# Kernel optimization log

Measured on AMD Instinct MI355X. Metric: run time of the kernel, lower is better.

Reference implementation:

```python
import jax, jax.numpy as jnp
import numpy as np

N = 50000          # num nodes
E = 800000         # num edges (avg degree 16)
C_IN = 64          # input channels
TOWERS = 4
F_IN = C_IN // TOWERS       # 16 (divide_input=True)
OUT = 128
F_OUT = OUT // TOWERS       # 32
NUM_AGG = 4                 # mean, std, max, min
NUM_SC = 3                  # identity, amplification, attenuation
AVG_LOG_DEG = float(np.log(17.0))  # deg histogram: all nodes degree 16 -> log(16+1)


def setup_inputs() -> dict:
    key = jax.random.key(0)
    ks = jax.random.split(key, 10)
    nodes = jax.random.normal(ks[0], (N, C_IN), dtype=jnp.float32)
    senders = jax.random.randint(ks[1], (E,), 0, N)
    receivers = jax.random.randint(ks[2], (E,), 0, N)
    # per-tower pre-MLP: Linear(2*F_IN -> F_IN), pre_layers=1 (no activation)
    pre_w = jax.random.normal(ks[3], (TOWERS, 2 * F_IN, F_IN), dtype=jnp.float32) / np.sqrt(2 * F_IN)
    pre_b = jnp.zeros((TOWERS, F_IN), dtype=jnp.float32)
    # per-tower post-MLP: Linear(F_IN + F_IN*12 -> F_OUT), post_layers=1
    post_in = F_IN + F_IN * NUM_AGG * NUM_SC  # 208
    post_w = jax.random.normal(ks[4], (TOWERS, post_in, F_OUT), dtype=jnp.float32) / np.sqrt(post_in)
    post_b = jnp.zeros((TOWERS, F_OUT), dtype=jnp.float32)
    # final linear: TOWERS*F_OUT -> OUT
    lin_w = jax.random.normal(ks[5], (TOWERS * F_OUT, OUT), dtype=jnp.float32) / np.sqrt(TOWERS * F_OUT)
    lin_b = jnp.zeros((OUT,), dtype=jnp.float32)
    return {"nodes": nodes, "senders": senders, "receivers": receivers,
            "pre_w": pre_w, "pre_b": pre_b, "post_w": post_w, "post_b": post_b,
            "lin_w": lin_w, "lin_b": lin_b}


def reference(nodes, senders, receivers, pre_w, pre_b, post_w, post_b, lin_w, lin_b):
    # divide_input=True: split channels across towers -> [N, T, F_IN]
    x = nodes.reshape(N, TOWERS, F_IN)
    x_i = x[senders]                                  # [E, T, F_IN]
    x_j = x[receivers]                                # [E, T, F_IN]
    h = jnp.concatenate([x_i, x_j], axis=-1)          # [E, T, 2*F_IN]
    # per-tower pre-MLP (single linear), vectorized over towers
    msg = jnp.einsum('etf,tfo->eto', h, pre_w) + pre_b  # [E, T, F_IN]

    # degree-scaled multi-aggregator segment reduce over receivers
    count = jax.ops.segment_sum(jnp.ones((E,), dtype=msg.dtype), receivers, num_segments=N)  # [N]
    d = jnp.clip(count, 1.0, None)
    inv_d = (1.0 / d)[:, None, None]
    mean = jax.ops.segment_sum(msg, receivers, num_segments=N) * inv_d           # [N,T,F]
    mean_sq = jax.ops.segment_sum(msg * msg, receivers, num_segments=N) * inv_d
    std = jnp.sqrt(jax.nn.relu(mean_sq - mean * mean) + 1e-5)
    has_nb = (count > 0)[:, None, None]
    mx = jax.ops.segment_max(msg, receivers, num_segments=N)
    mx = jnp.where(has_nb, mx, 0.0)
    mn = -jax.ops.segment_max(-msg, receivers, num_segments=N)
    mn = jnp.where(has_nb, mn, 0.0)
    agg = jnp.concatenate([mean, std, mx, mn], axis=-1)  # [N, T, 4*F_IN]

    # scalers: identity, amplification, attenuation (degree clamped to >= 1)
    log_d = jnp.log(d + 1.0)[:, None, None]
    amp = log_d / AVG_LOG_DEG
    att = AVG_LOG_DEG / log_d
    scaled = jnp.concatenate([agg, agg * amp, agg * att], axis=-1)  # [N, T, 12*F_IN]

    out = jnp.concatenate([x, scaled], axis=-1)                     # [N, T, 13*F_IN]
    outs = jnp.einsum('ntf,tfo->nto', out, post_w) + post_b         # [N, T, F_OUT]
    flat = outs.reshape(N, TOWERS * F_OUT)                          # [N, 128]
    return flat @ lin_w + lin_b                                     # [N, OUT]
```

## Files before the change

### kernel.cpp

```cpp
#include <hip/hip_runtime.h>

#define AVG_LOG_DEG 2.8332133440562162f
#define CAP 64

typedef __attribute__((ext_vector_type(8))) short short8;
typedef __attribute__((ext_vector_type(4))) float f32x4;

static __device__ __forceinline__ float bl(unsigned u) { return __uint_as_float(u << 16); }
static __device__ __forceinline__ float bh(unsigned u) { return __uint_as_float(u & 0xffff0000u); }
static __device__ __forceinline__ unsigned short f2b(float f) {
    unsigned u = __float_as_uint(f);
    return (unsigned short)((u + 0x7fffu + ((u >> 16) & 1u)) >> 16);
}
static __device__ __forceinline__ unsigned pk(unsigned short lo, unsigned short hi) {
    return (unsigned)lo | ((unsigned)hi << 16);
}


__global__ __launch_bounds__(256) void k_setup(
    const float* __restrict__ nodes, const float* __restrict__ pre_w,
    const float* __restrict__ post_w, const float* __restrict__ lin_w,
    float* __restrict__ Y, unsigned short* __restrict__ postT,
    unsigned short* __restrict__ linT, int* __restrict__ cursor,
    int n, int A, int nbN)
{
    int b = blockIdx.x;
    if (b < A) {
        int lane = threadIdx.x & 63;
        int node = b * 4 + (threadIdx.x >> 6);
        if (node >= n) return;
        int t = lane >> 4, f = lane & 15;
        float w[16];
        #pragma unroll
        for (int k = 0; k < 16; ++k)
            w[k] = pre_w[(t * 32 + k) * 16 + f];
        const float4* xp = reinterpret_cast<const float4*>(nodes + (size_t)node * 64 + t * 16);
        float4 x0 = xp[0], x1 = xp[1], x2 = xp[2], x3 = xp[3];
        float xs[16] = {x0.x, x0.y, x0.z, x0.w, x1.x, x1.y, x1.z, x1.w,
                        x2.x, x2.y, x2.z, x2.w, x3.x, x3.y, x3.z, x3.w};
        float y = 0.f;
        #pragma unroll
        for (int k = 0; k < 16; ++k)
            y = fmaf(xs[k], w[k], y);
        Y[(size_t)node * 64 + lane] = y;
    } else if (b < A + 176) {
        int i = (b - A) * 256 + threadIdx.x;
        if (i < 28672) {
            int t = i / (32 * 224);
            int r = i % (32 * 224);
            int nn = r / 224;
            int k = r % 224;
            float wv;
            if (k < 192)      wv = post_w[((size_t)t * 208 + 16 + k) * 32 + nn];
            else if (k < 208) wv = post_w[((size_t)t * 208 + (k - 192)) * 32 + nn];
            else              wv = 0.f;
            postT[i] = f2b(wv);
        }
        int j = i - 28672;
        if (j >= 0 && j < 16384) {
            int nn = j >> 7, k = j & 127;
            linT[j] = f2b(lin_w[k * 128 + nn]);
        }
    } else {
        int i = (b - A - 176) * 256 + threadIdx.x;
        if (i < n) cursor[i] = 0;
    }
}


__global__ __launch_bounds__(256) void k_scatter2(
    const int* __restrict__ send, const int* __restrict__ recv,
    int* __restrict__ cursor, int* __restrict__ slots,
    int e, int nps)
{
    int slice = blockIdx.x & 7;
    int chunk = blockIdx.x >> 3;
    int base = chunk * 2048;
    int lo = slice * nps;
    #pragma unroll
    for (int it = 0; it < 8; ++it) {
        int i = base + it * 256 + threadIdx.x;
        if (i < e) {
            int r = recv[i];
            if ((unsigned)(r - lo) < (unsigned)nps) {
                int p = atomicAdd(&cursor[r], 1);
                if (p < CAP) slots[(size_t)r * CAP + p] = send[i];
            }
        }
    }
}


__global__ __launch_bounds__(256) void k_agg(
    const float* __restrict__ nodes,
    const float* __restrict__ pre_w,
    const float* __restrict__ pre_b,
    const int* __restrict__ cursor,
    const int* __restrict__ slots, const float* __restrict__ Y,
    unsigned short* __restrict__ aggh, int n)
{
    int lane = threadIdx.x & 63;
    int node = blockIdx.x * 4 + (threadIdx.x >> 6);
    if (node >= n) return;
    int t = lane >> 4, f = lane & 15;

    int idxv = slots[(size_t)node * CAP + lane];

    float w[16];
    #pragma unroll
    for (int k = 0; k < 16; ++k)
        w[k] = pre_w[(t * 32 + 16 + k) * 16 + f];
    const float4* xp = reinterpret_cast<const float4*>(nodes + (size_t)node * 64 + t * 16);
    float4 x0 = xp[0], x1 = xp[1], x2 = xp[2], x3 = xp[3];
    float xs[16] = {x0.x, x0.y, x0.z, x0.w, x1.x, x1.y, x1.z, x1.w,
                    x2.x, x2.y, x2.z, x2.w, x3.x, x3.y, x3.z, x3.w};
    float hjw = pre_b[t * 16 + f];
    #pragma unroll
    for (int k = 0; k < 16; ++k)
        hjw = fmaf(xs[k], w[k], hjw);

    int d = min(cursor[node], CAP);
    const float* Yl = Y + lane;

    float s = 0.f, s2 = 0.f, mx = -INFINITY, mn = INFINITY;
    int e = 0;
    for (; e + 16 <= d; e += 16) {
        float v[16];
        #pragma unroll
        for (int q = 0; q < 16; ++q) {
            int si = __builtin_amdgcn_readlane(idxv, e + q);
            v[q] = Yl[(size_t)si * 64];
        }
        #pragma unroll
        for (int q = 0; q < 16; ++q) {
            float m = v[q] + hjw;
            s += m;
            s2 = fmaf(m, m, s2);
            mx = fmaxf(mx, m);
            mn = fminf(mn, m);
        }
    }
    int rem = d - e;
    if (rem > 0) {
        float v[16];
        #pragma unroll
        for (int q = 0; q < 16; ++q) {
            int si = __builtin_amdgcn_readlane(idxv, min(e + q, d - 1));
            v[q] = Yl[(size_t)si * 64];
        }
        #pragma unroll
        for (int q = 0; q < 16; ++q) {
            if (q < rem) {
                float m = v[q] + hjw;
                s += m;
                s2 = fmaf(m, m, s2);
                mx = fmaxf(mx, m);
                mn = fminf(mn, m);
            }
        }
    }

    float dc = fmaxf((float)d, 1.f);
    float inv = 1.f / dc;
    float mean = s * inv;
    float var = fmaf(-mean, mean, s2 * inv);
    float sd = sqrtf(fmaxf(var, 0.f) + 1e-5f);
    if (d == 0) { mx = 0.f; mn = 0.f; }

    unsigned short* ag = aggh + (size_t)node * 256 + t * 64 + f;
    ag[0]  = f2b(mean);
    ag[16] = f2b(sd);
    ag[32] = f2b(mx);
    ag[48] = f2b(mn);
}


__global__ __launch_bounds__(256, 3) void k_post(
    const float* __restrict__ nodes,
    const unsigned short* __restrict__ aggh,
    const int* __restrict__ deg,
    const unsigned short* __restrict__ postT,
    const unsigned short* __restrict__ linT,
    const float* __restrict__ post_b,
    const float* __restrict__ lin_b,
    float* __restrict__ out, int n)
{
    __shared__ unsigned short sV[32 * 256];
    __shared__ unsigned short sFlat[32 * 128];
    __shared__ float sAmp[32], sAtt[32];

    int tid = threadIdx.x;
    int n0 = blockIdx.x * 32;

    if (tid < 32) {
        int g = min(n0 + tid, n - 1);
        float dc = fmaxf((float)min(deg[g], CAP), 1.f);
        float ld = logf(dc + 1.f);
        sAmp[tid] = ld * (1.f / AVG_LOG_DEG);
        sAtt[tid] = AVG_LOG_DEG / ld;
    }

    int w = tid >> 6, lane = tid & 63;
    int quad = lane >> 4, mr = lane & 15;
    int mstrip = w & 1, nhalf = w >> 1;
    int nn = tid >> 3, j8 = tid & 7;
    int sw = nn & 7;
    int gn = min(n0 + nn, n - 1);
    int rsw = mr & 7;

    uint4 pa4[4];
    #pragma unroll
    for (int t = 0; t < 4; ++t)
        pa4[t] = *reinterpret_cast<const uint4*>(aggh + (size_t)gn * 256 + t * 64 + j8 * 8);

    uint4 xw4[4];
    #pragma unroll
    for (int t = 0; t < 4; ++t) { xw4[t].x = 0; xw4[t].y = 0; xw4[t].z = 0; xw4[t].w = 0; }
    if (j8 < 2) {
        #pragma unroll
        for (int t = 0; t < 4; ++t) {
            const float4* xp = reinterpret_cast<const float4*>(nodes + (size_t)gn * 64 + t * 16 + j8 * 8);
            float4 xa = xp[0], xb = xp[1];
            xw4[t].x = pk(f2b(xa.x), f2b(xa.y)); xw4[t].y = pk(f2b(xa.z), f2b(xa.w));
            xw4[t].z = pk(f2b(xb.x), f2b(xb.y)); xw4[t].w = pk(f2b(xb.z), f2b(xb.w));
        }
    }

    const unsigned short* bbase = postT + (size_t)(nhalf * 16 + mr) * 224 + quad * 8;
    short8 bA[7], bB[7];
    #pragma unroll
    for (int kk = 0; kk < 7; ++kk) bA[kk] = *reinterpret_cast<const short8*>(bbase + kk * 32);
    #pragma unroll
    for (int kk = 0; kk < 7; ++kk) bB[kk] = *reinterpret_cast<const short8*>(bbase + 32 * 224 + kk * 32);

    __syncthreads();
    float ampv = sAmp[nn], attv = sAtt[nn];

    #pragma unroll
    for (int t = 0; t < 4; ++t) {
        {
            unsigned short* row = &sV[nn * 256];
            uint4 a = pa4[t];
            *reinterpret_cast<uint4*>(row + (j8 ^ sw) * 8) = a;
            unsigned uu[4] = {a.x, a.y, a.z, a.w};
            unsigned short pa[8], pb[8];
            #pragma unroll
            for (int q = 0; q < 4; ++q) {
                float lo = bl(uu[q]), hi = bh(uu[q]);
                pa[2*q]   = f2b(lo * ampv); pa[2*q+1] = f2b(hi * ampv);
                pb[2*q]   = f2b(lo * attv); pb[2*q+1] = f2b(hi * attv);
            }
            uint4 wa, wb;
            wa.x = pk(pa[0], pa[1]); wa.y = pk(pa[2], pa[3]);
            wa.z = pk(pa[4], pa[5]); wa.w = pk(pa[6], pa[7]);
            wb.x = pk(pb[0], pb[1]); wb.y = pk(pb[2], pb[3]);
            wb.z = pk(pb[4], pb[5]); wb.w = pk(pb[6], pb[7]);
            *reinterpret_cast<uint4*>(row + (8  + (j8 ^ sw)) * 8) = wa;
            *reinterpret_cast<uint4*>(row + (16 + (j8 ^ sw)) * 8) = wb;
            *reinterpret_cast<uint4*>(row + (24 + (j8 ^ sw)) * 8) = xw4[t];
        }
        __syncthreads();

        f32x4 acc = {0.f, 0.f, 0.f, 0.f};
        const unsigned short* av0 = &sV[(mstrip * 16 + mr) * 256];
        #pragma unroll
        for (int kk = 0; kk < 7; ++kk) {
            int c = kk * 4 + quad;
            int pc = (c & ~7) | ((c & 7) ^ rsw);
            short8 avv = *reinterpret_cast<const short8*>(av0 + pc * 8);
            if (t & 1) acc = __builtin_amdgcn_mfma_f32_16x16x32_bf16(avv, bB[kk], acc, 0, 0, 0);
            else       acc = __builtin_amdgcn_mfma_f32_16x16x32_bf16(avv, bA[kk], acc, 0, 0, 0);
        }

        if (t == 0) {
            #pragma unroll
            for (int kk = 0; kk < 7; ++kk)
                bA[kk] = *reinterpret_cast<const short8*>(bbase + 2 * 32 * 224 + kk * 32);
        } else if (t == 1) {
            #pragma unroll
            for (int kk = 0; kk < 7; ++kk)
                bB[kk] = *reinterpret_cast<const short8*>(bbase + 3 * 32 * 224 + kk * 32);
        }

        int col = t * 32 + nhalf * 16 + mr;
        float pbv = post_b[col];
        int cc = col >> 3, co = col & 7;
        #pragma unroll
        for (int i = 0; i < 4; ++i) {
            int rowf = mstrip * 16 + quad * 4 + i;
            int pc = (cc & ~7) | ((cc & 7) ^ (rowf & 7));
            sFlat[rowf * 128 + pc * 8 + co] = f2b(acc[i] + pbv);
        }
        __syncthreads();
    }

    f32x4 facc[4];
    #pragma unroll
    for (int nt = 0; nt < 4; ++nt) { facc[nt].x = 0.f; facc[nt].y = 0.f; facc[nt].z = 0.f; facc[nt].w = 0.f; }

    const unsigned short* af0 = &sFlat[(mstrip * 16 + mr) * 128];
    #pragma unroll
    for (int kk = 0; kk < 4; ++kk) {
        int c = kk * 4 + quad;
        int pc = (c & ~7) | ((c & 7) ^ rsw);
        short8 avv = *reinterpret_cast<const short8*>(af0 + pc * 8);
        #pragma unroll
        for (int nt = 0; nt < 4; ++nt) {
            short8 bv = *reinterpret_cast<const short8*>(
                linT + (size_t)(nhalf * 64 + nt * 16 + mr) * 128 + kk * 32 + quad * 8);
            facc[nt] = __builtin_amdgcn_mfma_f32_16x16x32_bf16(avv, bv, facc[nt], 0, 0, 0);
        }
    }

    #pragma unroll
    for (int nt = 0; nt < 4; ++nt) {
        int col = nhalf * 64 + nt * 16 + mr;
        float lb = lin_b[col];
        #pragma unroll
        for (int i = 0; i < 4; ++i) {
            int node = n0 + mstrip * 16 + quad * 4 + i;
            if (node < n) out[(size_t)node * 128 + col] = facc[nt][i] + lb;
        }
    }
}

extern "C" void kernel_launch(void* const* d_in, const int* in_sizes, int n_in,
                              void* d_out, int out_size, void* d_ws, size_t ws_size,
                              hipStream_t stream)
{
    const float* nodes  = (const float*)d_in[0];
    const int*   send   = (const int*)d_in[1];
    const int*   recv   = (const int*)d_in[2];
    const float* pre_w  = (const float*)d_in[3];
    const float* pre_b  = (const float*)d_in[4];
    const float* post_w = (const float*)d_in[5];
    const float* post_b = (const float*)d_in[6];
    const float* lin_w  = (const float*)d_in[7];
    const float* lin_b  = (const float*)d_in[8];
    float* out = (float*)d_out;

    int N = in_sizes[0] / 64;
    int E = in_sizes[1];
    int Npad = (N + 255) & ~255;

    int* cursor = (int*)d_ws;
    int* slots  = cursor + Npad;
    float* Y    = (float*)(slots + (size_t)Npad * CAP);
    unsigned short* aggh  = (unsigned short*)(Y + (size_t)Npad * 64);
    unsigned short* postT = aggh + (size_t)Npad * 256;
    unsigned short* linT  = postT + 28672;

    int nbN = (N + 255) / 256;
    int A = (N + 3) / 4;
    int nps = (N + 7) / 8;
    int nbS = 8 * ((E + 2047) / 2048);

    k_setup   <<<A + 176 + nbN, 256, 0, stream>>>(nodes, pre_w, post_w, lin_w,
                                                  Y, postT, linT, cursor, N, A, nbN);
    k_scatter2<<<nbS, 256, 0, stream>>>(send, recv, cursor, slots, E, nps);
    k_agg     <<<(N + 3) / 4, 256, 0, stream>>>(nodes, pre_w, pre_b, cursor, slots, Y, aggh, N);
    k_post    <<<(N + 31) / 32, 256, 0, stream>>>(nodes, aggh, cursor, postT, linT,
                                                  post_b, lin_b, out, N);
}
```

Before: 201.5 us.

## Store gathered projections in bf16, precompute receiver term, vectorize scatter loads

The setup kernel now computes both halves of the pre-MLP. It stores the sender projection as bf16 (Yh) and the receiver projection plus bias as fp32 (H), so the aggregation kernel no longer recomputes the receiver term. This halves the bytes of the random per-edge gathers in k_agg. The scatter kernel now loads receiver indices as int4 with 4096 edges per chunk. The cost is bf16 rounding of the message inputs before they are reduced with mean, std, max and min, plus an extra H buffer write and read.

Result: slower. 206.5 us (+2.5%).

```diff
diff --git a/kernel.cpp b/kernel.cpp
--- a/kernel.cpp
+++ b/kernel.cpp
@@ -19,8 +19,10 @@
 
 __global__ __launch_bounds__(256) void k_setup(
     const float* __restrict__ nodes, const float* __restrict__ pre_w,
+    const float* __restrict__ pre_b,
     const float* __restrict__ post_w, const float* __restrict__ lin_w,
-    float* __restrict__ Y, unsigned short* __restrict__ postT,
+    unsigned short* __restrict__ Yh, float* __restrict__ H,
+    unsigned short* __restrict__ postT,
     unsigned short* __restrict__ linT, int* __restrict__ cursor,
     int n, int A, int nbN)
 {
@@ -30,19 +32,25 @@
         int node = b * 4 + (threadIdx.x >> 6);
         if (node >= n) return;
         int t = lane >> 4, f = lane & 15;
-        float w[16];
-        #pragma unroll
-        for (int k = 0; k < 16; ++k)
-            w[k] = pre_w[(t * 32 + k) * 16 + f];
+        float w0[16], w1[16];
+        #pragma unroll
+        for (int k = 0; k < 16; ++k) {
+            w0[k] = pre_w[(t * 32 + k) * 16 + f];
+            w1[k] = pre_w[(t * 32 + 16 + k) * 16 + f];
+        }
         const float4* xp = reinterpret_cast<const float4*>(nodes + (size_t)node * 64 + t * 16);
         float4 x0 = xp[0], x1 = xp[1], x2 = xp[2], x3 = xp[3];
         float xs[16] = {x0.x, x0.y, x0.z, x0.w, x1.x, x1.y, x1.z, x1.w,
                         x2.x, x2.y, x2.z, x2.w, x3.x, x3.y, x3.z, x3.w};
         float y = 0.f;
-        #pragma unroll
-        for (int k = 0; k < 16; ++k)
-            y = fmaf(xs[k], w[k], y);
-        Y[(size_t)node * 64 + lane] = y;
+        float h = pre_b[t * 16 + f];
+        #pragma unroll
+        for (int k = 0; k < 16; ++k) {
+            y = fmaf(xs[k], w0[k], y);
+            h = fmaf(xs[k], w1[k], h);
+        }
+        Yh[(size_t)node * 64 + lane] = f2b(y);
+        H[(size_t)node * 64 + lane] = h;
     } else if (b < A + 176) {
         int i = (b - A) * 256 + threadIdx.x;
         if (i < 28672) {
@@ -75,16 +83,31 @@
 {
     int slice = blockIdx.x & 7;
     int chunk = blockIdx.x >> 3;
-    int base = chunk * 2048;
+    int base = chunk * 4096 + threadIdx.x * 4;
     int lo = slice * nps;
-    #pragma unroll
-    for (int it = 0; it < 8; ++it) {
-        int i = base + it * 256 + threadIdx.x;
-        if (i < e) {
-            int r = recv[i];
+    int4 rv[4];
+    #pragma unroll
+    for (int it = 0; it < 4; ++it) {
+        int i = base + it * 1024;
+        if (i + 3 < e) {
+            rv[it] = *reinterpret_cast<const int4*>(recv + i);
+        } else {
+            rv[it].x = rv[it].y = rv[it].z = rv[it].w = -1;
+            #pragma unroll
+            for (int q = 0; q < 4; ++q)
+                if (i + q < e) ((int*)&rv[it])[q] = recv[i + q];
+        }
+    }
+    #pragma unroll
+    for (int it = 0; it < 4; ++it) {
+        int i = base + it * 1024;
+        int rr[4] = {rv[it].x, rv[it].y, rv[it].z, rv[it].w};
+        #pragma unroll
+        for (int q = 0; q < 4; ++q) {
+            int r = rr[q];
             if ((unsigned)(r - lo) < (unsigned)nps) {
                 int p = atomicAdd(&cursor[r], 1);
-                if (p < CAP) slots[(size_t)r * CAP + p] = send[i];
+                if (p < CAP) slots[(size_t)r * CAP + p] = send[i + q];
             }
         }
     }
@@ -92,11 +115,10 @@
 
 
 __global__ __launch_bounds__(256) void k_agg(
-    const float* __restrict__ nodes,
-    const float* __restrict__ pre_w,
-    const float* __restrict__ pre_b,
     const int* __restrict__ cursor,
-    const int* __restrict__ slots, const float* __restrict__ Y,
+    const int* __restrict__ slots,
+    const unsigned short* __restrict__ Yh,
+    const float* __restrict__ H,
     unsigned short* __restrict__ aggh, int n)
 {
     int lane = threadIdx.x & 63;
@@ -105,27 +127,14 @@
     int t = lane >> 4, f = lane & 15;
 
     int idxv = slots[(size_t)node * CAP + lane];
-
-    float w[16];
-    #pragma unroll
-    for (int k = 0; k < 16; ++k)
-        w[k] = pre_w[(t * 32 + 16 + k) * 16 + f];
-    const float4* xp = reinterpret_cast<const float4*>(nodes + (size_t)node * 64 + t * 16);
-    float4 x0 = xp[0], x1 = xp[1], x2 = xp[2], x3 = xp[3];
-    float xs[16] = {x0.x, x0.y, x0.z, x0.w, x1.x, x1.y, x1.z, x1.w,
-                    x2.x, x2.y, x2.z, x2.w, x3.x, x3.y, x3.z, x3.w};
-    float hjw = pre_b[t * 16 + f];
-    #pragma unroll
-    for (int k = 0; k < 16; ++k)
-        hjw = fmaf(xs[k], w[k], hjw);
-
+    float hjw = H[(size_t)node * 64 + lane];
     int d = min(cursor[node], CAP);
-    const float* Yl = Y + lane;
+    const unsigned short* Yl = Yh + lane;
 
     float s = 0.f, s2 = 0.f, mx = -INFINITY, mn = INFINITY;
     int e = 0;
     for (; e + 16 <= d; e += 16) {
-        float v[16];
+        unsigned v[16];
         #pragma unroll
         for (int q = 0; q < 16; ++q) {
             int si = __builtin_amdgcn_readlane(idxv, e + q);
@@ -133,7 +142,7 @@
         }
         #pragma unroll
         for (int q = 0; q < 16; ++q) {
-            float m = v[q] + hjw;
+            float m = __uint_as_float(v[q] << 16) + hjw;
             s += m;
             s2 = fmaf(m, m, s2);
             mx = fmaxf(mx, m);
@@ -142,7 +151,7 @@
     }
     int rem = d - e;
     if (rem > 0) {
-        float v[16];
+        unsigned v[16];
         #pragma unroll
         for (int q = 0; q < 16; ++q) {
             int si = __builtin_amdgcn_readlane(idxv, min(e + q, d - 1));
@@ -151,7 +160,7 @@
         #pragma unroll
         for (int q = 0; q < 16; ++q) {
             if (q < rem) {
-                float m = v[q] + hjw;
+                float m = __uint_as_float(v[q] << 16) + hjw;
                 s += m;
                 s2 = fmaf(m, m, s2);
                 mx = fmaxf(mx, m);
@@ -345,20 +354,21 @@
 
     int* cursor = (int*)d_ws;
     int* slots  = cursor + Npad;
-    float* Y    = (float*)(slots + (size_t)Npad * CAP);
-    unsigned short* aggh  = (unsigned short*)(Y + (size_t)Npad * 64);
+    unsigned short* Yh = (unsigned short*)(slots + (size_t)Npad * CAP);
+    float* H = (float*)(Yh + (size_t)Npad * 64);
+    unsigned short* aggh  = (unsigned short*)(H + (size_t)Npad * 64);
     unsigned short* postT = aggh + (size_t)Npad * 256;
     unsigned short* linT  = postT + 28672;
 
     int nbN = (N + 255) / 256;
     int A = (N + 3) / 4;
     int nps = (N + 7) / 8;
-    int nbS = 8 * ((E + 2047) / 2048);
-
-    k_setup   <<<A + 176 + nbN, 256, 0, stream>>>(nodes, pre_w, post_w, lin_w,
-                                                  Y, postT, linT, cursor, N, A, nbN);
+    int nbS = 8 * ((E + 4095) / 4096);
+
+    k_setup   <<<A + 176 + nbN, 256, 0, stream>>>(nodes, pre_w, pre_b, post_w, lin_w,
+                                                  Yh, H, postT, linT, cursor, N, A, nbN);
     k_scatter2<<<nbS, 256, 0, stream>>>(send, recv, cursor, slots, E, nps);
-    k_agg     <<<(N + 3) / 4, 256, 0, stream>>>(nodes, pre_w, pre_b, cursor, slots, Y, aggh, N);
+    k_agg     <<<(N + 3) / 4, 256, 0, stream>>>(cursor, slots, Yh, H, aggh, N);
     k_post    <<<(N + 31) / 32, 256, 0, stream>>>(nodes, aggh, cursor, postT, linT,
                                                   post_b, lin_b, out, N);
 }
```
